# Kernel tuning notes

Measured on AMD Instinct MI355X. Metric: run time of the kernel, lower is better.

The kernel has to match this reference:

```python
import jax, jax.numpy as jnp
import numpy as np

TOP_K = 8
ROUTE_SCALE = 2.5
NUM_EXPERTS = 64


def setup_inputs() -> dict:
    key = jax.random.key(0)
    k1, k2, k3 = jax.random.split(key, 3)
    x = jax.random.normal(k1, (16384, 4096), dtype=jnp.float32)
    gate_weight = jax.random.normal(k2, (NUM_EXPERTS, 4096), dtype=jnp.float32) * 0.02
    expert_bias = jax.random.normal(k3, (NUM_EXPERTS,), dtype=jnp.float32) * 0.01
    return {"x": x, "gate_weight": gate_weight, "expert_bias": expert_bias}


def reference(x, gate_weight, expert_bias):
    # gate linear: [T, dim] @ [dim, E] -> [T, E]
    logits = jnp.einsum("td,ed->te", x, gate_weight)
    scores = jax.nn.sigmoid(logits.astype(jnp.float32))  # score_func == 'sigmoid'
    # expert_bias branch: top-k over biased scores, gather unbiased scores
    _, selected_experts_indices = jax.lax.top_k(scores + expert_bias[None, :], TOP_K)
    top_scores = jnp.take_along_axis(scores, selected_experts_indices, axis=1)
    # route_norm (sigmoid normalization)
    denom = top_scores.sum(axis=-1, keepdims=True) + 1e-20
    top_scores = top_scores / denom * ROUTE_SCALE
    # histogram over selected expert indices (torch.histc returns float)
    flat_idx = selected_experts_indices.reshape(-1)
    num_tokens_per_expert = jnp.zeros((NUM_EXPERTS,), jnp.float32).at[flat_idx].add(1.0)
    return top_scores, selected_experts_indices, num_tokens_per_expert
```

## Files before the change

kernel.cpp:

```cpp
#include <hip/hip_runtime.h>
#include <math.h>

#define NTOK 16384
#define DIM  4096
#define NE   64
#define TOPK 8
#define SPLITK 8
#define NSPW 16
#define ROUTE_SCALE 2.5f

typedef __attribute__((ext_vector_type(8))) short short8v;
typedef __attribute__((ext_vector_type(4))) float f32x4;

__device__ __forceinline__ void split3_pack(const float* v, uint4& b0, uint4& b1, uint4& b2)
{
    uint p0[8], p1[8], p2[8];
#pragma unroll
    for (int j = 0; j < 8; ++j) {
        const float xv = v[j];
        const uint  u0 = __float_as_uint(xv) & 0xffff0000u;
        const float f0 = __uint_as_float(u0);
        const float r  = xv - f0;
        const uint  u1 = __float_as_uint(r) & 0xffff0000u;
        const float f1 = __uint_as_float(u1);
        const float r2 = r - f1;
        const uint  u2 = __float_as_uint(r2) & 0xffff0000u;
        p0[j] = u0; p1[j] = u1; p2[j] = u2;
    }
    b0 = make_uint4(p0[1] | (p0[0] >> 16), p0[3] | (p0[2] >> 16),
                    p0[5] | (p0[4] >> 16), p0[7] | (p0[6] >> 16));
    b1 = make_uint4(p1[1] | (p1[0] >> 16), p1[3] | (p1[2] >> 16),
                    p1[5] | (p1[4] >> 16), p1[7] | (p1[6] >> 16));
    b2 = make_uint4(p2[1] | (p2[0] >> 16), p2[3] | (p2[2] >> 16),
                    p2[5] | (p2[4] >> 16), p2[7] | (p2[6] >> 16));
}

__global__ __launch_bounds__(256)
void prep_w(const float* __restrict__ gw, uint4* __restrict__ wS)
{
    const int tid  = blockIdx.x * 256 + threadIdx.x;
    const int lane = tid & 63;
    const int nt   = (tid >> 6) & 3;
    const int ks   = tid >> 8;
    const int e    = nt * 16 + (lane & 15);
    const int kb   = ks * 32 + (lane >> 4) * 8;
    float v[8];
    *(float4*)&v[0] = *(const float4*)&gw[(size_t)e * DIM + kb];
    *(float4*)&v[4] = *(const float4*)&gw[(size_t)e * DIM + kb + 4];
    uint4 b0, b1, b2;
    split3_pack(v, b0, b1, b2);
    const size_t base = (size_t)(ks * 4 + nt) * 3 * 64 + lane;
    wS[base] = b0; wS[base + 64] = b1; wS[base + 128] = b2;
}

__device__ __forceinline__ void gld_lds16(const float* g, float* l)
{
    __builtin_amdgcn_global_load_lds(
        (const __attribute__((address_space(1))) unsigned int*)g,
        (__attribute__((address_space(3))) unsigned int*)l,
        16, 0, 0);
}

#define MFMA6(A0, A1, A2, B0, B1, B2, ACC) do {                              \
    ACC = __builtin_amdgcn_mfma_f32_16x16x32_bf16(A2, B0, ACC, 0, 0, 0);     \
    ACC = __builtin_amdgcn_mfma_f32_16x16x32_bf16(A1, B1, ACC, 0, 0, 0);     \
    ACC = __builtin_amdgcn_mfma_f32_16x16x32_bf16(A0, B2, ACC, 0, 0, 0);     \
    ACC = __builtin_amdgcn_mfma_f32_16x16x32_bf16(A1, B0, ACC, 0, 0, 0);     \
    ACC = __builtin_amdgcn_mfma_f32_16x16x32_bf16(A0, B1, ACC, 0, 0, 0);     \
    ACC = __builtin_amdgcn_mfma_f32_16x16x32_bf16(A0, B0, ACC, 0, 0, 0);     \
} while (0)

#define SB __builtin_amdgcn_sched_barrier(0)
#define WAITV(N) do { SB; asm volatile("s_waitcnt vmcnt(" #N ")" ::: "memory"); SB; } while (0)

__global__ __launch_bounds__(512, 4)
void router_fused(const float* __restrict__ x, const uint4* __restrict__ wS,
                  const float* __restrict__ bias, float* __restrict__ out)
{
    __shared__ float pool[SPLITK * 2 * 1024];
    __shared__ int   hist[NE];

    const int t    = threadIdx.x;
    const int lane = t & 63;
    const int wv   = __builtin_amdgcn_readfirstlane(t >> 6);
    const int r15  = lane & 15;
    const int g    = lane >> 4;
    const int tok0 = blockIdx.x * 32;
    const int ks0  = wv * NSPW;

    if (t < NE) hist[t] = 0;

    const int lr  = lane >> 3;
    const int swz = (lane & 7) ^ lr;
    const float* gsrc0 = x + (size_t)(tok0 +  0 + lr) * DIM + ks0 * 32 + swz * 4;
    const float* gsrc1 = x + (size_t)(tok0 +  8 + lr) * DIM + ks0 * 32 + swz * 4;
    const float* gsrc2 = x + (size_t)(tok0 + 16 + lr) * DIM + ks0 * 32 + swz * 4;
    const float* gsrc3 = x + (size_t)(tok0 + 24 + lr) * DIM + ks0 * 32 + swz * 4;

    const uint4* wq = wS + lane;

    f32x4 acc[4][2];
#pragma unroll
    for (int nt = 0; nt < 4; ++nt) {
        acc[nt][0] = (f32x4){0.f, 0.f, 0.f, 0.f};
        acc[nt][1] = (f32x4){0.f, 0.f, 0.f, 0.f};
    }
    uint4 B[12];

    const int jr = r15 >> 3;
    const int R  = r15 & 7;
    const int q0 = (2 * g) ^ R;
    const int q1 = (2 * g + 1) ^ R;

#define DMAC(c) do {                                                         \
        float* ldst = &pool[(size_t)(wv * 2 + ((c) & 1)) * 1024];            \
        gld_lds16(gsrc0 + (size_t)(c) * 32, ldst);                           \
        gld_lds16(gsrc1 + (size_t)(c) * 32, ldst + 256);                     \
        gld_lds16(gsrc2 + (size_t)(c) * 32, ldst + 512);                     \
        gld_lds16(gsrc3 + (size_t)(c) * 32, ldst + 768);                     \
    } while (0)
#define LOADB(cg) do {                                                       \
        const size_t sgb = (size_t)(ks0 + (cg)) * 768;                       \
        _Pragma("unroll")                                                    \
        for (int nt = 0; nt < 4; ++nt)                                       \
            _Pragma("unroll")                                                \
            for (int sp = 0; sp < 3; ++sp)                                   \
                B[nt * 3 + sp] = wq[sgb + nt * 192 + sp * 64];               \
    } while (0)

    LOADB(0);
    DMAC(0);
    DMAC(1);

#pragma unroll 1
    for (int c = 0; c < NSPW; ++c) {
        if (c == NSPW - 1) { WAITV(0); } else { WAITV(4); }
        {
            const float* sbase = &pool[(size_t)(wv * 2 + (c & 1)) * 1024];
            float a8[8]; uint4 u0, u1, u2;
            *(float4*)&a8[0] = *(const float4*)&sbase[jr * 256 + R * 32 + q0 * 4];
            *(float4*)&a8[4] = *(const float4*)&sbase[jr * 256 + R * 32 + q1 * 4];
            split3_pack(a8, u0, u1, u2);
            const short8v A0h0 = *(short8v*)&u0, A1h0 = *(short8v*)&u1, A2h0 = *(short8v*)&u2;
            *(float4*)&a8[0] = *(const float4*)&sbase[(jr + 2) * 256 + R * 32 + q0 * 4];
            *(float4*)&a8[4] = *(const float4*)&sbase[(jr + 2) * 256 + R * 32 + q1 * 4];
            split3_pack(a8, u0, u1, u2);
            const short8v A0h1 = *(short8v*)&u0, A1h1 = *(short8v*)&u1, A2h1 = *(short8v*)&u2;
#pragma unroll
            for (int nt = 0; nt < 4; ++nt) {
                MFMA6(A0h0, A1h0, A2h0, *(const short8v*)&B[nt * 3 + 0],
                      *(const short8v*)&B[nt * 3 + 1], *(const short8v*)&B[nt * 3 + 2],
                      acc[nt][0]);
                MFMA6(A0h1, A1h1, A2h1, *(const short8v*)&B[nt * 3 + 0],
                      *(const short8v*)&B[nt * 3 + 1], *(const short8v*)&B[nt * 3 + 2],
                      acc[nt][1]);
            }
        }
        SB;
        if (c + 1 < NSPW) LOADB(c + 1);
        SB;
        if (c + 2 < NSPW) DMAC(c + 2);
        SB;
    }
#undef DMAC
#undef LOADB

    float (*part)[32][NE] = (float (*)[32][NE])pool;
#pragma unroll
    for (int nt = 0; nt < 4; ++nt)
#pragma unroll
        for (int G = 0; G < 2; ++G)
#pragma unroll
            for (int q = 0; q < 4; ++q)
                part[wv][G * 16 + g * 4 + q][nt * 16 + r15] = acc[nt][G][q];

    __syncthreads();

    const float bias_l = bias[lane];
#pragma unroll 1
    for (int i = 0; i < 4; ++i) {
        const int tok = wv * 4 + i;
        float logit = 0.f;
#pragma unroll
        for (int kh = 0; kh < SPLITK; ++kh)
            logit += part[kh][tok][lane];
        const float s = 1.f / (1.f + expf(-logit));
        float myv  = s + bias_l;
        float outv = 0.f;
        int   outi = 0;
        float sum  = 0.f;
#pragma unroll
        for (int k = 0; k < TOPK; ++k) {
            float cv = myv;
            int   ci = lane;
#pragma unroll
            for (int off = 32; off; off >>= 1) {
                float ov = __shfl_xor(cv, off, 64);
                int   oi = __shfl_xor(ci, off, 64);
                if (ov > cv || (ov == cv && oi < ci)) { cv = ov; ci = oi; }
            }
            float ts = __shfl(s, ci, 64);
            sum += ts;
            if (lane == k)  { outv = ts; outi = ci; }
            if (lane == ci) { myv = -1e30f; }
        }
        const float denom = sum + 1e-20f;
        const size_t gt = (size_t)tok0 + tok;
        if (lane < TOPK) {
            out[gt * TOPK + lane] = (outv / denom) * ROUTE_SCALE;
            out[(size_t)NTOK * TOPK + gt * TOPK + lane] = (float)outi;
            atomicAdd(&hist[outi], 1);
        }
    }

    __syncthreads();
    if (t < NE) {
        int cgt = hist[t];
        if (cgt) atomicAdd(&out[(size_t)NTOK * TOPK * 2 + t], (float)cgt);
    }
}

extern "C" void kernel_launch(void* const* d_in, const int* in_sizes, int n_in,
                              void* d_out, int out_size, void* d_ws, size_t ws_size,
                              hipStream_t stream)
{
    const float* x    = (const float*)d_in[0];
    const float* gw   = (const float*)d_in[1];
    const float* bias = (const float*)d_in[2];
    float* out = (float*)d_out;
    uint4* wS  = (uint4*)d_ws;

    hipMemsetAsync(out + (size_t)NTOK * TOPK * 2, 0, NE * sizeof(float), stream);

    prep_w<<<128, 256, 0, stream>>>(gw, wS);
    router_fused<<<NTOK / 32, 512, 0, stream>>>(x, wS, bias, out);
}
```

Measured before the change: 97.44 us.

## Interleave per-tile B loads with MFMA phases using fine-grained vmcnt waits

Splits the B-fragment global load into four per-n-tile groups issued right after the MFMA phase that consumes the same registers. vmcnt waits are tuned so each phase only waits for the loads it needs, which removes the scheduling barriers. Wraps MFMA bursts in s_setprio to favour matrix issue across waves. The last iteration is peeled with draining wait counts. This overlaps memory latency with compute, but it depends on exact vmcnt counting, and a wrong count would give a race.

```diff
diff --git a/kernel.cpp b/kernel.cpp
--- a/kernel.cpp
+++ b/kernel.cpp
@@ -119,51 +119,60 @@
         gld_lds16(gsrc2 + (size_t)(c) * 32, ldst + 512);                     \
         gld_lds16(gsrc3 + (size_t)(c) * 32, ldst + 768);                     \
     } while (0)
-#define LOADB(cg) do {                                                       \
-        const size_t sgb = (size_t)(ks0 + (cg)) * 768;                       \
-        _Pragma("unroll")                                                    \
-        for (int nt = 0; nt < 4; ++nt)                                       \
-            _Pragma("unroll")                                                \
-            for (int sp = 0; sp < 3; ++sp)                                   \
-                B[nt * 3 + sp] = wq[sgb + nt * 192 + sp * 64];               \
+#define LOADBNT(nt, cg) do {                                                 \
+        const size_t sgb = (size_t)(ks0 + (cg)) * 768 + (nt) * 192;          \
+        B[(nt) * 3 + 0] = wq[sgb];                                           \
+        B[(nt) * 3 + 1] = wq[sgb + 64];                                      \
+        B[(nt) * 3 + 2] = wq[sgb + 128];                                     \
     } while (0)
-
-    LOADB(0);
+#define APREP(c)                                                             \
+        const float* sbase = &pool[(size_t)(wv * 2 + ((c) & 1)) * 1024];     \
+        float a8[8]; uint4 u0, u1, u2;                                       \
+        *(float4*)&a8[0] = *(const float4*)&sbase[jr * 256 + R * 32 + q0 * 4];       \
+        *(float4*)&a8[4] = *(const float4*)&sbase[jr * 256 + R * 32 + q1 * 4];       \
+        split3_pack(a8, u0, u1, u2);                                         \
+        const short8v A0h0 = *(short8v*)&u0, A1h0 = *(short8v*)&u1, A2h0 = *(short8v*)&u2; \
+        *(float4*)&a8[0] = *(const float4*)&sbase[(jr + 2) * 256 + R * 32 + q0 * 4]; \
+        *(float4*)&a8[4] = *(const float4*)&sbase[(jr + 2) * 256 + R * 32 + q1 * 4]; \
+        split3_pack(a8, u0, u1, u2);                                         \
+        const short8v A0h1 = *(short8v*)&u0, A1h1 = *(short8v*)&u1, A2h1 = *(short8v*)&u2;
+#define PHASE(nt) do {                                                       \
+        __builtin_amdgcn_s_setprio(1);                                       \
+        MFMA6(A0h0, A1h0, A2h0, *(const short8v*)&B[(nt)*3+0],               \
+              *(const short8v*)&B[(nt)*3+1], *(const short8v*)&B[(nt)*3+2],  \
+              acc[nt][0]);                                                   \
+        MFMA6(A0h1, A1h1, A2h1, *(const short8v*)&B[(nt)*3+0],               \
+              *(const short8v*)&B[(nt)*3+1], *(const short8v*)&B[(nt)*3+2],  \
+              acc[nt][1]);                                                   \
+        __builtin_amdgcn_s_setprio(0);                                       \
+    } while (0)
+
     DMAC(0);
+    LOADBNT(0, 0); LOADBNT(1, 0); LOADBNT(2, 0); LOADBNT(3, 0);
     DMAC(1);
 
 #pragma unroll 1
-    for (int c = 0; c < NSPW; ++c) {
-        if (c == NSPW - 1) { WAITV(0); } else { WAITV(4); }
-        {
-            const float* sbase = &pool[(size_t)(wv * 2 + (c & 1)) * 1024];
-            float a8[8]; uint4 u0, u1, u2;
-            *(float4*)&a8[0] = *(const float4*)&sbase[jr * 256 + R * 32 + q0 * 4];
-            *(float4*)&a8[4] = *(const float4*)&sbase[jr * 256 + R * 32 + q1 * 4];
-            split3_pack(a8, u0, u1, u2);
-            const short8v A0h0 = *(short8v*)&u0, A1h0 = *(short8v*)&u1, A2h0 = *(short8v*)&u2;
-            *(float4*)&a8[0] = *(const float4*)&sbase[(jr + 2) * 256 + R * 32 + q0 * 4];
-            *(float4*)&a8[4] = *(const float4*)&sbase[(jr + 2) * 256 + R * 32 + q1 * 4];
-            split3_pack(a8, u0, u1, u2);
-            const short8v A0h1 = *(short8v*)&u0, A1h1 = *(short8v*)&u1, A2h1 = *(short8v*)&u2;
-#pragma unroll
-            for (int nt = 0; nt < 4; ++nt) {
-                MFMA6(A0h0, A1h0, A2h0, *(const short8v*)&B[nt * 3 + 0],
-                      *(const short8v*)&B[nt * 3 + 1], *(const short8v*)&B[nt * 3 + 2],
-                      acc[nt][0]);
-                MFMA6(A0h1, A1h1, A2h1, *(const short8v*)&B[nt * 3 + 0],
-                      *(const short8v*)&B[nt * 3 + 1], *(const short8v*)&B[nt * 3 + 2],
-                      acc[nt][1]);
-            }
-        }
-        SB;
-        if (c + 1 < NSPW) LOADB(c + 1);
-        SB;
+    for (int c = 0; c < NSPW - 1; ++c) {
+        WAITV(13);
+        APREP(c);
+        PHASE(0); LOADBNT(0, c + 1); WAITV(13);
+        PHASE(1); LOADBNT(1, c + 1); WAITV(13);
+        PHASE(2); LOADBNT(2, c + 1); WAITV(13);
+        PHASE(3); LOADBNT(3, c + 1);
         if (c + 2 < NSPW) DMAC(c + 2);
-        SB;
+    }
+    {
+        WAITV(9);
+        APREP(NSPW - 1);
+        PHASE(0); WAITV(6);
+        PHASE(1); WAITV(3);
+        PHASE(2); WAITV(0);
+        PHASE(3);
     }
 #undef DMAC
-#undef LOADB
+#undef LOADBNT
+#undef APREP
+#undef PHASE
 
     float (*part)[32][NE] = (float (*)[32][NE])pool;
 #pragma unroll
```

Result: faster. 94.73 us (-2.8%).
